# Kernel tuning notes

Measured on AMD Instinct MI355X. Metric: run time of the kernel, lower is better.

The kernel has to match this reference:

```python
import jax, jax.numpy as jnp
import numpy as np

B, S, H = 2, 2048, 2048
E, I, TOPK = 8, 1408, 2


def setup_inputs() -> dict:
    key = jax.random.key(0)
    k0, k1, k2, k3, k4 = jax.random.split(key, 5)
    return {
        "hidden_states": jax.random.normal(k0, (B, S, H), dtype=jnp.float32),
        "Wr": jax.random.normal(k1, (H, E), dtype=jnp.float32) * 0.02,
        "Wg": jax.random.normal(k2, (E, H, I), dtype=jnp.float32) * 0.02,
        "Wu": jax.random.normal(k3, (E, H, I), dtype=jnp.float32) * 0.02,
        "Wd": jax.random.normal(k4, (E, I, H), dtype=jnp.float32) * 0.02,
    }


def reference(hidden_states, Wr, Wg, Wu, Wd):
    b, s, h = hidden_states.shape
    x = hidden_states.reshape(-1, h)                      # [T, H]
    T = x.shape[0]
    router_logits = x @ Wr                                # [T, E]
    probs = jax.nn.softmax(router_logits.astype(jnp.float32), axis=-1)
    top_w, top_i = jax.lax.top_k(probs, TOPK)             # [T, k]
    top_w = top_w / jnp.sum(top_w, axis=-1, keepdims=True)  # norm_topk_prob
    top_w = top_w.astype(x.dtype)
    # combine weights per (token, expert): zero where expert not selected
    cw = jnp.zeros((T, E), dtype=x.dtype).at[
        jnp.arange(T)[:, None], top_i].add(top_w)         # [T, E]
    # per-expert SwiGLU MLP computed densely, masked/weighted by cw
    g = jax.nn.silu(jnp.einsum('th,ehi->tei', x, Wg))     # [T, E, I]
    u = jnp.einsum('th,ehi->tei', x, Wu)                  # [T, E, I]
    y = jnp.einsum('tei,eih->teh', g * u, Wd)             # [T, E, H]
    out = jnp.einsum('te,teh->th', cw, y)                 # [T, H]
    return out.reshape(b, s, h), router_logits
```

## Files before the change

### kernel.cpp

```cpp
#include <hip/hip_runtime.h>

#define T_TOK 4096
#define HD 2048
#define NE 8
#define NI 1408

typedef __bf16 bf16x8 __attribute__((ext_vector_type(8)));
typedef float f32x4 __attribute__((ext_vector_type(4)));
typedef unsigned short ushort8 __attribute__((ext_vector_type(8)));

#define S_WAITCNT_VMCNT(n) asm volatile("s_waitcnt vmcnt(" #n ")" ::: "memory")
__device__ __forceinline__ void wave_barrier() {
  asm volatile("" ::: "memory");
  __builtin_amdgcn_s_barrier();
  asm volatile("" ::: "memory");
}

__device__ __forceinline__ unsigned short f2bf(float f) {
  unsigned int u = __float_as_uint(f);
  u += 0x7FFFu + ((u >> 16) & 1u);
  return (unsigned short)(u >> 16);
}
__device__ __forceinline__ float bf2f(unsigned short u) {
  return __uint_as_float((unsigned int)u << 16);
}

__device__ __forceinline__ void gload_lds16(const void* g, void* l) {
  __builtin_amdgcn_global_load_lds(
      (const __attribute__((address_space(1))) unsigned int*)g,
      (__attribute__((address_space(3))) unsigned int*)l, 16, 0, 0);
}

__global__ void transpose_cvt2_kernel(const float* __restrict__ srcA,
                                      unsigned short* __restrict__ dstA,
                                      const float* __restrict__ srcB,
                                      unsigned short* __restrict__ dstB,
                                      int R, int C, int dual) {
  int z = blockIdx.z;
  int e = dual ? (z >> 1) : z;
  const float* sp = (dual && (z & 1)) ? srcB : srcA;
  unsigned short* dp = (dual && (z & 1)) ? dstB : dstA;
  int c0 = blockIdx.x * 64, r0 = blockIdx.y * 128;
  const float* s = sp + (size_t)e * R * C;
  unsigned short* d = dp + (size_t)e * R * C;
  int tid = threadIdx.x;
  int tj = tid & 15, ti = tid >> 4;
  const float* sb = s + (size_t)(r0 + ti * 8) * C + c0 + tj * 4;
  f32x4 v[8];
#pragma unroll
  for (int r = 0; r < 8; r++) v[r] = *(const f32x4*)(sb + (size_t)r * C);
  unsigned short* db = d + (size_t)(c0 + tj * 4) * R + r0 + ti * 8;
#pragma unroll
  for (int cc = 0; cc < 4; cc++) {
    ushort8 o;
#pragma unroll
    for (int r = 0; r < 8; r++) o[r] = f2bf(v[r][cc]);
    *(ushort8*)(db + (size_t)cc * R) = o;
  }
}

__global__ void router_kernel(const float* __restrict__ x,
                              const float* __restrict__ Wr,
                              float* __restrict__ logits,
                              unsigned short* __restrict__ xbf,
                              int4* __restrict__ tokinfo,
                              int* __restrict__ cnt) {
  int wv = threadIdx.x >> 6, lane = threadIdx.x & 63;
  int t = blockIdx.x * 4 + wv;
  const float* xr = x + (size_t)t * HD;
  unsigned short* xbr = xbf + (size_t)t * HD;
  float acc[NE];
#pragma unroll
  for (int e = 0; e < NE; e++) acc[e] = 0.f;
  for (int hi = 0; hi < HD / 256; hi++) {
    int h = hi * 256 + lane * 4;
    f32x4 xv = *(const f32x4*)(xr + h);
    ushort4 o = { f2bf(xv[0]), f2bf(xv[1]), f2bf(xv[2]), f2bf(xv[3]) };
    *(ushort4*)(xbr + h) = o;
#pragma unroll
    for (int j = 0; j < 4; j++) {
      const float4* w4 = (const float4*)(Wr + (size_t)(h + j) * NE);
      float4 a = w4[0], b = w4[1];
      float xs = xv[j];
      acc[0] += xs * a.x; acc[1] += xs * a.y; acc[2] += xs * a.z; acc[3] += xs * a.w;
      acc[4] += xs * b.x; acc[5] += xs * b.y; acc[6] += xs * b.z; acc[7] += xs * b.w;
    }
  }
#pragma unroll
  for (int m = 32; m > 0; m >>= 1) {
#pragma unroll
    for (int e = 0; e < NE; e++) acc[e] += __shfl_xor(acc[e], m, 64);
  }
  if (lane < NE) logits[(size_t)t * NE + lane] = acc[lane];
  if (lane == 0) {
    int e0 = 0;
#pragma unroll
    for (int e = 1; e < NE; e++) if (acc[e] > acc[e0]) e0 = e;
    int e1 = (e0 == 0) ? 1 : 0;
#pragma unroll
    for (int e = 0; e < NE; e++) if (e != e0 && acc[e] > acc[e1]) e1 = e;
    float ex = expf(acc[e1] - acc[e0]);
    float w0 = 1.f / (1.f + ex);
    float w1 = ex / (1.f + ex);
    atomicAdd(&cnt[e0], 1);
    atomicAdd(&cnt[e1], 1);
    tokinfo[t] = make_int4(e0, e1, __float_as_int(w0), __float_as_int(w1));
  }
}

__global__ void offsets_kernel(int* __restrict__ cnt) {
  int o = 0;
  for (int e = 0; e < NE; e++) { cnt[8 + e] = o; o += cnt[e]; }
}

__global__ void scatter_kernel(const int4* __restrict__ tokinfo,
                               int* __restrict__ cnt,
                               int* __restrict__ row_tok,
                               int2* __restrict__ tok2row) {
  int t = blockIdx.x * blockDim.x + threadIdx.x;
  if (t >= T_TOK) return;
  int4 info = tokinfo[t];
  int p0 = atomicAdd(&cnt[16 + info.x], 1);
  int r0 = cnt[8 + info.x] + p0;
  row_tok[r0] = t;
  int p1 = atomicAdd(&cnt[16 + info.y], 1);
  int r1 = cnt[8 + info.y] + p1;
  row_tok[r1] = t;
  tok2row[t] = make_int2(r0, r1);
}

__launch_bounds__(256, 2)
__global__ void gemm1_kernel(const unsigned short* __restrict__ xbf,
                             const unsigned short* __restrict__ Wgt,
                             const unsigned short* __restrict__ Wut,
                             unsigned short* __restrict__ act,
                             const int* __restrict__ row_tok,
                             const int* __restrict__ cnt) {
  const int f = blockIdx.x + 11 * (blockIdx.y + 32 * blockIdx.z);
  const int e = f & 7;
  const int rem = f >> 3;
  const int nt = rem >> 5;
  const int mt = rem & 31;
  const int c = cnt[e];
  if (mt * 128 >= c) return;
  const int off = cnt[8 + e];
  const int rowbase = off + mt * 128, rowend = off + c;
  const int i0 = nt * 128;
  __shared__ __align__(16) char smem[49152];
  const int lane = threadIdx.x & 63, w = threadIdx.x >> 6;
  const int wr = w >> 1, wc = w & 1;

  const int rr0 = w * 16 + (lane >> 2);
  const int rr1 = rr0 + 64;
  const int q0 = (lane & 3) ^ ((rr0 >> 1) & 3);
  const int q1 = (lane & 3) ^ ((rr1 >> 1) & 3);
  int g0 = rowbase + rr0; if (g0 > rowend - 1) g0 = rowend - 1;
  int g1 = rowbase + rr1; if (g1 > rowend - 1) g1 = rowend - 1;
  const size_t tokA0 = (size_t)row_tok[g0] * HD;
  const size_t tokA1 = (size_t)row_tok[g1] * HD;
  const size_t bB0 = ((size_t)e * NI + i0 + rr0) * HD;
  const size_t bB1 = ((size_t)e * NI + i0 + rr1) * HD;
  const int ldsA = w * 1024;

  f32x4 zero = {0.f, 0.f, 0.f, 0.f};
  f32x4 accg[4][4], accu[4][4];
#pragma unroll
  for (int a = 0; a < 4; a++)
#pragma unroll
    for (int b = 0; b < 4; b++) { accg[a][b] = zero; accu[a][b] = zero; }

  auto stage = [&](int buf, int ks) {
    const int k0 = ks * 32;
    char* base = smem + buf * 24576;
    gload_lds16(xbf + tokA0 + k0 + q0 * 8, base + ldsA);
    gload_lds16(xbf + tokA1 + k0 + q1 * 8, base + ldsA + 4096);
    gload_lds16(Wgt + bB0 + k0 + q0 * 8, base + 8192 + ldsA);
    gload_lds16(Wgt + bB1 + k0 + q1 * 8, base + 8192 + ldsA + 4096);
    gload_lds16(Wut + bB0 + k0 + q0 * 8, base + 16384 + ldsA);
    gload_lds16(Wut + bB1 + k0 + q1 * 8, base + 16384 + ldsA + 4096);
  };
  const int rl = lane & 15, kslot = lane >> 4;
  auto compute = [&](int buf) {
    const char* base = smem + buf * 24576;
    bf16x8 af[4], bg[4], bu[4];
#pragma unroll
    for (int mi = 0; mi < 4; mi++) {
      int r = wr * 64 + mi * 16 + rl;
      int byt = r * 64 + ((kslot ^ ((r >> 1) & 3)) << 4);
      af[mi] = *(const bf16x8*)(base + byt);
    }
#pragma unroll
    for (int ni = 0; ni < 4; ni++) {
      int r = wc * 64 + ni * 16 + rl;
      int byt = r * 64 + ((kslot ^ ((r >> 1) & 3)) << 4);
      bg[ni] = *(const bf16x8*)(base + 8192 + byt);
      bu[ni] = *(const bf16x8*)(base + 16384 + byt);
    }
#pragma unroll
    for (int mi = 0; mi < 4; mi++)
#pragma unroll
      for (int ni = 0; ni < 4; ni++) {
        accg[mi][ni] = __builtin_amdgcn_mfma_f32_16x16x32_bf16(af[mi], bg[ni], accg[mi][ni], 0, 0, 0);
        accu[mi][ni] = __builtin_amdgcn_mfma_f32_16x16x32_bf16(af[mi], bu[ni], accu[mi][ni], 0, 0, 0);
      }
  };

  stage(0, 0);
  const int NKS = HD / 32;
  int ks = 0;
  for (; ks < NKS - 1; ks++) {
    stage((ks + 1) & 1, ks + 1);
    S_WAITCNT_VMCNT(6);
    wave_barrier();
    compute(ks & 1);
    wave_barrier();
  }
  S_WAITCNT_VMCNT(0);
  wave_barrier();
  compute(ks & 1);

  const int rh = lane >> 4;
#pragma unroll
  for (int mi = 0; mi < 4; mi++)
#pragma unroll
    for (int ni = 0; ni < 4; ni++)
#pragma unroll
      for (int j = 0; j < 4; j++) {
        int grow = rowbase + wr * 64 + mi * 16 + rh * 4 + j;
        if (grow < rowend) {
          int gcol = i0 + wc * 64 + ni * 16 + rl;
          float g = accg[mi][ni][j], u = accu[mi][ni][j];
          float val = g / (1.f + __expf(-g)) * u;
          act[(size_t)grow * NI + gcol] = f2bf(val);
        }
      }
}

__launch_bounds__(256, 3)
__global__ void gemm2_kernel(const unsigned short* __restrict__ act,
                             const unsigned short* __restrict__ Wdt,
                             unsigned short* __restrict__ y,
                             const int* __restrict__ cnt) {
  const int f = blockIdx.x + 16 * (blockIdx.y + 32 * blockIdx.z);
  const int e = f & 7;
  const int rem = f >> 3;
  const int nt = rem >> 5;
  const int mt = rem & 31;
  const int c = cnt[e];
  if (mt * 128 >= c) return;
  const int off = cnt[8 + e];
  const int rowbase = off + mt * 128, rowend = off + c;
  const int n0 = nt * 128;
  __shared__ __align__(16) char smem[32768];
  const int lane = threadIdx.x & 63, w = threadIdx.x >> 6;
  const int wr = w >> 1, wc = w & 1;

  const int rr0 = w * 16 + (lane >> 2);
  const int rr1 = rr0 + 64;
  const int q0 = (lane & 3) ^ ((rr0 >> 1) & 3);
  const int q1 = (lane & 3) ^ ((rr1 >> 1) & 3);
  int g0 = rowbase + rr0; if (g0 > rowend - 1) g0 = rowend - 1;
  int g1 = rowbase + rr1; if (g1 > rowend - 1) g1 = rowend - 1;
  const size_t aA0 = (size_t)g0 * NI;
  const size_t aA1 = (size_t)g1 * NI;
  const size_t bB0 = ((size_t)e * HD + n0 + rr0) * NI;
  const size_t bB1 = ((size_t)e * HD + n0 + rr1) * NI;
  const int ldsA = w * 1024;

  f32x4 zero = {0.f, 0.f, 0.f, 0.f};
  f32x4 acc[4][4];
#pragma unroll
  for (int a = 0; a < 4; a++)
#pragma unroll
    for (int b = 0; b < 4; b++) acc[a][b] = zero;

  auto stage = [&](int buf, int ks) {
    const int k0 = ks * 32;
    char* base = smem + buf * 16384;
    gload_lds16(act + aA0 + k0 + q0 * 8, base + ldsA);
    gload_lds16(act + aA1 + k0 + q1 * 8, base + ldsA + 4096);
    gload_lds16(Wdt + bB0 + k0 + q0 * 8, base + 8192 + ldsA);
    gload_lds16(Wdt + bB1 + k0 + q1 * 8, base + 8192 + ldsA + 4096);
  };
  const int rl = lane & 15, kslot = lane >> 4;
  auto compute = [&](int buf) {
    const char* base = smem + buf * 16384;
    bf16x8 af[4], bf[4];
#pragma unroll
    for (int mi = 0; mi < 4; mi++) {
      int r = wr * 64 + mi * 16 + rl;
      int byt = r * 64 + ((kslot ^ ((r >> 1) & 3)) << 4);
      af[mi] = *(const bf16x8*)(base + byt);
    }
#pragma unroll
    for (int ni = 0; ni < 4; ni++) {
      int r = wc * 64 + ni * 16 + rl;
      int byt = r * 64 + ((kslot ^ ((r >> 1) & 3)) << 4);
      bf[ni] = *(const bf16x8*)(base + 8192 + byt);
    }
#pragma unroll
    for (int mi = 0; mi < 4; mi++)
#pragma unroll
      for (int ni = 0; ni < 4; ni++)
        acc[mi][ni] = __builtin_amdgcn_mfma_f32_16x16x32_bf16(af[mi], bf[ni], acc[mi][ni], 0, 0, 0);
  };

  stage(0, 0);
  const int NKS = NI / 32;
  int ks = 0;
  for (; ks < NKS - 1; ks++) {
    stage((ks + 1) & 1, ks + 1);
    S_WAITCNT_VMCNT(4);
    wave_barrier();
    compute(ks & 1);
    wave_barrier();
  }
  S_WAITCNT_VMCNT(0);
  wave_barrier();
  compute(ks & 1);

  const int rh = lane >> 4;
#pragma unroll
  for (int mi = 0; mi < 4; mi++)
#pragma unroll
    for (int ni = 0; ni < 4; ni++)
#pragma unroll
      for (int j = 0; j < 4; j++) {
        int grow = rowbase + wr * 64 + mi * 16 + rh * 4 + j;
        if (grow < rowend) {
          int gcol = n0 + wc * 64 + ni * 16 + rl;
          y[(size_t)grow * HD + gcol] = f2bf(acc[mi][ni][j]);
        }
      }
}

__global__ void combine_kernel(const unsigned short* __restrict__ y,
                               const int2* __restrict__ tok2row,
                               const int4* __restrict__ tokinfo,
                               float* __restrict__ out) {
  int t = blockIdx.x, tid = threadIdx.x;
  int2 rr = tok2row[t];
  int4 info = tokinfo[t];
  float w0 = __int_as_float(info.z), w1 = __int_as_float(info.w);
  ushort8 a = ((const ushort8*)(y + (size_t)rr.x * HD))[tid];
  ushort8 b = ((const ushort8*)(y + (size_t)rr.y * HD))[tid];
  float4 o0, o1;
  o0.x = w0 * bf2f(a[0]) + w1 * bf2f(b[0]);
  o0.y = w0 * bf2f(a[1]) + w1 * bf2f(b[1]);
  o0.z = w0 * bf2f(a[2]) + w1 * bf2f(b[2]);
  o0.w = w0 * bf2f(a[3]) + w1 * bf2f(b[3]);
  o1.x = w0 * bf2f(a[4]) + w1 * bf2f(b[4]);
  o1.y = w0 * bf2f(a[5]) + w1 * bf2f(b[5]);
  o1.z = w0 * bf2f(a[6]) + w1 * bf2f(b[6]);
  o1.w = w0 * bf2f(a[7]) + w1 * bf2f(b[7]);
  float4* op = (float4*)(out + (size_t)t * HD + tid * 8);
  op[0] = o0; op[1] = o1;
}

extern "C" void kernel_launch(void* const* d_in, const int* in_sizes, int n_in,
                              void* d_out, int out_size, void* d_ws, size_t ws_size,
                              hipStream_t stream) {
  const float* x  = (const float*)d_in[0];
  const float* Wr = (const float*)d_in[1];
  const float* Wg = (const float*)d_in[2];
  const float* Wu = (const float*)d_in[3];
  const float* Wd = (const float*)d_in[4];
  float* out = (float*)d_out;
  char* ws = (char*)d_ws;

  unsigned short* xbf = (unsigned short*)(ws);
  unsigned short* Wgt = (unsigned short*)(ws + 16777216);
  unsigned short* Wut = (unsigned short*)(ws + 62914560);
  unsigned short* Wdt = (unsigned short*)(ws + 109051904);
  unsigned short* act = (unsigned short*)(ws + 155189248);
  unsigned short* yb  = (unsigned short*)(ws + 16777216);
  int4*  tokinfo      = (int4*)(ws + 178257920);
  int*   row_tok      = (int*)(ws + 178323456);
  int2*  tok2row      = (int2*)(ws + 178356224);
  int*   cnt          = (int*)(ws + 178388992);

  hipMemsetAsync(cnt, 0, 128, stream);

  router_kernel<<<T_TOK / 4, 256, 0, stream>>>(x, Wr, out + (size_t)T_TOK * HD, xbf, tokinfo, cnt);
  offsets_kernel<<<1, 1, 0, stream>>>(cnt);
  scatter_kernel<<<T_TOK / 256, 256, 0, stream>>>(tokinfo, cnt, row_tok, tok2row);

  transpose_cvt2_kernel<<<dim3(NI / 64, HD / 128, NE * 2), 256, 0, stream>>>(
      Wg, Wgt, Wu, Wut, HD, NI, 1);
  transpose_cvt2_kernel<<<dim3(HD / 64, NI / 128, NE), 256, 0, stream>>>(
      Wd, Wdt, nullptr, nullptr, NI, HD, 0);

  gemm1_kernel<<<dim3(11, 32, NE), 256, 0, stream>>>(xbf, Wgt, Wut, act, row_tok, cnt);
  gemm2_kernel<<<dim3(16, 32, NE), 256, 0, stream>>>(act, Wdt, yb, cnt);
  combine_kernel<<<T_TOK, 256, 0, stream>>>(yb, tok2row, tokinfo, out);
}
```

Before: 472.8 us.

## Triple-buffer GEMM K-loop prefetch and merge offset/scatter kernels

Both expert GEMM kernels move from a double-buffered to a triple-buffered LDS pipeline, staging two K-slices ahead and adjusting vmcnt waits so more global loads are in flight during compute. The offsets and scatter kernels are fused into a single one-block kernel to remove a launch. The larger shared memory (72KB for gemm1, 48KB for gemm2) may reduce occupancy below the launch_bounds targets, and the single-block scatter serializes the routing work.

```diff
diff --git a/kernel.cpp b/kernel.cpp
--- a/kernel.cpp
+++ b/kernel.cpp
@@ -108,25 +108,25 @@
   }
 }
 
-__global__ void offsets_kernel(int* __restrict__ cnt) {
-  int o = 0;
-  for (int e = 0; e < NE; e++) { cnt[8 + e] = o; o += cnt[e]; }
-}
-
-__global__ void scatter_kernel(const int4* __restrict__ tokinfo,
-                               int* __restrict__ cnt,
-                               int* __restrict__ row_tok,
-                               int2* __restrict__ tok2row) {
-  int t = blockIdx.x * blockDim.x + threadIdx.x;
-  if (t >= T_TOK) return;
-  int4 info = tokinfo[t];
-  int p0 = atomicAdd(&cnt[16 + info.x], 1);
-  int r0 = cnt[8 + info.x] + p0;
-  row_tok[r0] = t;
-  int p1 = atomicAdd(&cnt[16 + info.y], 1);
-  int r1 = cnt[8 + info.y] + p1;
-  row_tok[r1] = t;
-  tok2row[t] = make_int2(r0, r1);
+__global__ void route_finalize_kernel(const int4* __restrict__ tokinfo,
+                                      int* __restrict__ cnt,
+                                      int* __restrict__ row_tok,
+                                      int2* __restrict__ tok2row) {
+  if (threadIdx.x == 0) {
+    int o = 0;
+    for (int e = 0; e < NE; e++) { cnt[8 + e] = o; o += cnt[e]; }
+  }
+  __syncthreads();
+  for (int t = threadIdx.x; t < T_TOK; t += 1024) {
+    int4 info = tokinfo[t];
+    int p0 = atomicAdd(&cnt[16 + info.x], 1);
+    int r0 = cnt[8 + info.x] + p0;
+    row_tok[r0] = t;
+    int p1 = atomicAdd(&cnt[16 + info.y], 1);
+    int r1 = cnt[8 + info.y] + p1;
+    row_tok[r1] = t;
+    tok2row[t] = make_int2(r0, r1);
+  }
 }
 
 __launch_bounds__(256, 2)
@@ -146,7 +146,7 @@
   const int off = cnt[8 + e];
   const int rowbase = off + mt * 128, rowend = off + c;
   const int i0 = nt * 128;
-  __shared__ __align__(16) char smem[49152];
+  __shared__ __align__(16) char smem[73728];
   const int lane = threadIdx.x & 63, w = threadIdx.x >> 6;
   const int wr = w >> 1, wc = w & 1;
 
@@ -206,18 +206,21 @@
   };
 
   stage(0, 0);
+  stage(1, 1);
   const int NKS = HD / 32;
-  int ks = 0;
-  for (; ks < NKS - 1; ks++) {
-    stage((ks + 1) & 1, ks + 1);
-    S_WAITCNT_VMCNT(6);
+  for (int ks = 0; ks < NKS; ks++) {
+    if (ks + 2 < NKS) {
+      stage((ks + 2) % 3, ks + 2);
+      S_WAITCNT_VMCNT(12);
+    } else if (ks + 1 < NKS) {
+      S_WAITCNT_VMCNT(6);
+    } else {
+      S_WAITCNT_VMCNT(0);
+    }
     wave_barrier();
-    compute(ks & 1);
+    compute(ks % 3);
     wave_barrier();
   }
-  S_WAITCNT_VMCNT(0);
-  wave_barrier();
-  compute(ks & 1);
 
   const int rh = lane >> 4;
 #pragma unroll
@@ -251,7 +254,7 @@
   const int off = cnt[8 + e];
   const int rowbase = off + mt * 128, rowend = off + c;
   const int n0 = nt * 128;
-  __shared__ __align__(16) char smem[32768];
+  __shared__ __align__(16) char smem[49152];
   const int lane = threadIdx.x & 63, w = threadIdx.x >> 6;
   const int wr = w >> 1, wc = w & 1;
 
@@ -306,18 +309,21 @@
   };
 
   stage(0, 0);
+  stage(1, 1);
   const int NKS = NI / 32;
-  int ks = 0;
-  for (; ks < NKS - 1; ks++) {
-    stage((ks + 1) & 1, ks + 1);
-    S_WAITCNT_VMCNT(4);
+  for (int ks = 0; ks < NKS; ks++) {
+    if (ks + 2 < NKS) {
+      stage((ks + 2) % 3, ks + 2);
+      S_WAITCNT_VMCNT(8);
+    } else if (ks + 1 < NKS) {
+      S_WAITCNT_VMCNT(4);
+    } else {
+      S_WAITCNT_VMCNT(0);
+    }
     wave_barrier();
-    compute(ks & 1);
+    compute(ks % 3);
     wave_barrier();
   }
-  S_WAITCNT_VMCNT(0);
-  wave_barrier();
-  compute(ks & 1);
 
   const int rh = lane >> 4;
 #pragma unroll
@@ -382,8 +388,7 @@
   hipMemsetAsync(cnt, 0, 128, stream);
 
   router_kernel<<<T_TOK / 4, 256, 0, stream>>>(x, Wr, out + (size_t)T_TOK * HD, xbf, tokinfo, cnt);
-  offsets_kernel<<<1, 1, 0, stream>>>(cnt);
-  scatter_kernel<<<T_TOK / 256, 256, 0, stream>>>(tokinfo, cnt, row_tok, tok2row);
+  route_finalize_kernel<<<1, 1024, 0, stream>>>(tokinfo, cnt, row_tok, tok2row);
 
   transpose_cvt2_kernel<<<dim3(NI / 64, HD / 128, NE * 2), 256, 0, stream>>>(
       Wg, Wgt, Wu, Wut, HD, NI, 1);
```

Result: faster. 462.0 us (-2.3%).
